# Kernel optimization log

Hardware: AMD Instinct MI355X
Metric: run time of the kernel (lower is better)

## Reference

```python
import jax, jax.numpy as jnp
import numpy as np

B, S, D, H, HID = 8192, 16, 128, 8, 1024
DH = D // H  # 16
GCN, NUMF = 40, 103
EPS = 1e-5

def _make_pe():
    pos = np.arange(S, dtype=np.float64)[:, None]
    i = np.arange(D, dtype=np.float64)[None, :]
    pe = pos / np.power(10000.0, (i // 2 * 2.0) / D)
    pe[:, 0::2] = np.sin(pe[:, 0::2])
    pe[:, 1::2] = np.cos(pe[:, 1::2])
    return jnp.asarray(pe, dtype=jnp.float32)  # [S, D]

PE = _make_pe()

def setup_inputs() -> dict:
    key = jax.random.key(0)
    ks = jax.random.split(key, 16)
    rn = lambda k, shape, s=0.02: (jax.random.normal(k, shape, jnp.float32) * s)
    return {
        "x": jax.random.normal(ks[0], (B, S, D), jnp.float32),
        "gcn_i": jax.random.normal(ks[1], (B, GCN), jnp.float32),
        "num": jax.random.normal(ks[2], (B, NUMF), jnp.float32),
        # two independent encoder layers, params stacked on leading dim
        "Wq": rn(ks[3], (2, D, D)), "bq": jnp.zeros((2, D), jnp.float32),
        "Wk": rn(ks[4], (2, D, D)), "bk": jnp.zeros((2, D), jnp.float32),
        "Wv": rn(ks[5], (2, D, D)), "bv": jnp.zeros((2, D), jnp.float32),
        "Wo": rn(ks[6], (2, D, D)), "bo": jnp.zeros((2, D), jnp.float32),
        "ln1_g": jnp.ones((2, D), jnp.float32), "ln1_b": jnp.zeros((2, D), jnp.float32),
        "W1": rn(ks[7], (2, D, HID)), "b1": jnp.zeros((2, HID), jnp.float32),
        "W2": rn(ks[8], (2, HID, D)), "b2": jnp.zeros((2, D), jnp.float32),
        "ln2_g": jnp.ones((2, D), jnp.float32), "ln2_b": jnp.zeros((2, D), jnp.float32),
        # head
        "Wn": rn(ks[9], (NUMF, D)), "bnum": jnp.zeros((D,), jnp.float32),
        "bn_gamma": jnp.ones((D,), jnp.float32), "bn_beta": jnp.zeros((D,), jnp.float32),
        "Wf": rn(ks[10], (S * D + GCN + D, 1)), "bf": jnp.zeros((1,), jnp.float32),
    }

def _ln(x, g, b):
    m = x.mean(-1, keepdims=True)
    v = ((x - m) ** 2).mean(-1, keepdims=True)
    return (x - m) * jax.lax.rsqrt(v + EPS) * g + b

def reference(x, gcn_i, num, Wq, bq, Wk, bk, Wv, bv, Wo, bo, ln1_g, ln1_b,
              W1, b1, W2, b2, ln2_g, ln2_b, Wn, bnum, bn_gamma, bn_beta, Wf, bf):
    out = x + PE  # positional encoding (dropout = identity in eval)
    scale = DH ** -0.5
    for l in range(2):
        # NOTE: original uses a raw .view(B*H, -1, DH) (no transpose) -- faithful reshape
        q = (out @ Wq[l] + bq[l]).reshape(B * H, S, DH)
        k = (out @ Wk[l] + bk[l]).reshape(B * H, S, DH)
        v = (out @ Wv[l] + bv[l]).reshape(B * H, S, DH)
        attn = jax.nn.softmax(jnp.einsum('nsd,ntd->nst', q, k) * scale, axis=-1)
        ctx = jnp.einsum('nst,ntd->nsd', attn, v).reshape(B, S, D)
        h = _ln(ctx @ Wo[l] + bo[l] + out, ln1_g[l], ln1_b[l])
        ff = jax.nn.relu(h @ W1[l] + b1[l]) @ W2[l] + b2[l]
        out = _ln(ff + h, ln2_g[l], ln2_b[l])
    flat = out.reshape(B, S * D)  # [B, 2048]
    n = num @ Wn + bnum  # [B, 128]
    # BatchNorm1d, training-mode forward (biased batch variance)
    mu = n.mean(0)
    var = ((n - mu) ** 2).mean(0)
    n = (n - mu) * jax.lax.rsqrt(var + EPS) * bn_gamma + bn_beta
    p = jnp.concatenate([flat, gcn_i, n], axis=-1)  # [B, 2216]
    return jax.nn.sigmoid(p @ Wf + bf)
```

## Files before the change

kernel.cpp:

```cpp
#include <hip/hip_runtime.h>
#include <hip/hip_bf16.h>
#include <math.h>

#define B_SZ   8192
#define S_SZ   16
#define D_SZ   128
#define HID_SZ 1024
#define NUMF_SZ 103
#define GCN_SZ 40
#define G_B    4
#define NBLK   (B_SZ / G_B)
#define STRD   136

typedef short bh8 __attribute__((ext_vector_type(8)));
typedef float fx4 __attribute__((ext_vector_type(4)));
typedef unsigned short us4 __attribute__((ext_vector_type(4)));

__device__ __forceinline__ fx4 mfma16(bh8 a, bh8 b, fx4 c) {
    return __builtin_amdgcn_mfma_f32_16x16x32_bf16(a, b, c, 0, 0, 0);
}

__device__ __forceinline__ unsigned short f2b(float f) {
    union { __hip_bfloat16 b; unsigned short u; } cv;
    cv.b = __float2bfloat16(f);
    return cv.u;
}
__device__ __forceinline__ float bu2f(unsigned short u) {
    return __uint_as_float(((unsigned)u) << 16);
}

__global__ __launch_bounds__(256) void prep_weights(
    const float* __restrict__ Wq, const float* __restrict__ Wk,
    const float* __restrict__ Wv, const float* __restrict__ Wo,
    const float* __restrict__ W1, const float* __restrict__ W2,
    unsigned short* __restrict__ WswQ, unsigned short* __restrict__ WswK,
    unsigned short* __restrict__ WswV, unsigned short* __restrict__ WswO,
    unsigned short* __restrict__ Wsw1, unsigned short* __restrict__ Wsw2,
    float* __restrict__ PEt)
{
    int j = blockIdx.x * 256 + threadIdx.x;
    if (j < 2048) {
        int s = j >> 7, c = j & 127;
        float expo = (float)((c >> 1) * 2) * (1.0f / 128.0f);
        float denom = powf(10000.0f, expo);
        float ang = (float)s / denom;
        PEt[j] = (c & 1) ? cosf(ang) : sinf(ang);
    }
    if (j < 2 * 16384) {
        int r = j & 16383, l = j >> 14;
        int k = r >> 7, n = r & 127;
        int dst = (((l * 8 + (n >> 4)) * 4 + (k >> 5)) * 64 +
                   (((k >> 3) & 3) * 16 + (n & 15))) * 8 + (k & 7);
        WswQ[dst] = f2b(Wq[j]); WswK[dst] = f2b(Wk[j]);
        WswV[dst] = f2b(Wv[j]); WswO[dst] = f2b(Wo[j]);
    }
    {
        int l = j >> 17, r = j & 131071;
        int k = r >> 10, n = r & 1023;
        int dst = (((l * 64 + (n >> 4)) * 4 + (k >> 5)) * 64 +
                   (((k >> 3) & 3) * 16 + (n & 15))) * 8 + (k & 7);
        Wsw1[dst] = f2b(W1[j]);
    }
    {
        int l = j >> 17, r = j & 131071;
        int k = r >> 7, n = r & 127;
        int dst = (((l * 8 + (n >> 4)) * 32 + (k >> 5)) * 64 +
                   (((k >> 3) & 3) * 16 + (n & 15))) * 8 + (k & 7);
        Wsw2[dst] = f2b(W2[j]);
    }
}

__global__ __launch_bounds__(256, 2) void encoder_fused(
    const float* __restrict__ x, const float* __restrict__ gcn,
    const float* __restrict__ bq, const float* __restrict__ bk,
    const float* __restrict__ bv, const float* __restrict__ bo,
    const float* __restrict__ ln1g, const float* __restrict__ ln1b,
    const float* __restrict__ b1, const float* __restrict__ b2p,
    const float* __restrict__ ln2g, const float* __restrict__ ln2b,
    const float* __restrict__ Wf,
    const unsigned short* __restrict__ WswQ, const unsigned short* __restrict__ WswK,
    const unsigned short* __restrict__ WswV, const unsigned short* __restrict__ WswO,
    const unsigned short* __restrict__ Wsw1, const unsigned short* __restrict__ Wsw2,
    const float* __restrict__ PEt,
    float* __restrict__ acc1)
{
    __shared__ unsigned short ACT[64][STRD];
    __shared__ unsigned short Qb[64][STRD];
    __shared__ unsigned short Kb[64][STRD];
    __shared__ unsigned short Vb[64][STRD];
    __shared__ float2 LNp2[64][4];
    __shared__ unsigned short Pb[4][16][16];

    unsigned short* Vb4 = &Vb[0][0];

    const int t = threadIdx.x;
    const int w = t >> 6, lane = t & 63;
    const int q = lane >> 4, ln = lane & 15;
    const int bbase = blockIdx.x * G_B;

    {
        const float4* xb = (const float4*)(x + (size_t)bbase * 2048);
        const float4* pe4 = (const float4*)PEt;
#pragma unroll
        for (int i = 0; i < 8; ++i) {
            int f4 = i * 256 + t;
            float4 xv = xb[f4];
            float4 pv = pe4[f4 & 511];
            int flat = f4 * 4;
            int row = flat >> 7, col = flat & 127;
            ushort4 pk = {f2b(xv.x + pv.x), f2b(xv.y + pv.y),
                          f2b(xv.z + pv.z), f2b(xv.w + pv.w)};
            *(ushort4*)&ACT[row][col] = pk;
        }
    }
    __syncthreads();

    for (int l = 0; l < 2; ++l) {
        {
            bh8 afr[4][4];
#pragma unroll
            for (int mt = 0; mt < 4; ++mt)
#pragma unroll
                for (int ks = 0; ks < 4; ++ks)
                    afr[mt][ks] = *(const bh8*)&ACT[mt * 16 + ln][ks * 32 + q * 8];
#pragma unroll
            for (int mtx = 0; mtx < 2; ++mtx) {
                const unsigned short* Wm = (mtx == 0) ? WswQ + l * 16384 : WswK + l * 16384;
                const float* bias = (mtx == 0) ? bq + l * 128 : bk + l * 128;
                unsigned short (*dst)[STRD] = (mtx == 0) ? Qb : Kb;
#pragma unroll
                for (int i2 = 0; i2 < 2; ++i2) {
                    int nt = w * 2 + i2;
                    bh8 wfr[4];
#pragma unroll
                    for (int ks = 0; ks < 4; ++ks)
                        wfr[ks] = *(const bh8*)(Wm + ((nt * 4 + ks) * 64 + lane) * 8);
                    int n0 = nt * 16 + q * 4;
                    fx4 bb4 = *(const fx4*)&bias[n0];
#pragma unroll
                    for (int mt = 0; mt < 4; ++mt) {
                        fx4 acc = {0.f, 0.f, 0.f, 0.f};
#pragma unroll
                        for (int ks = 0; ks < 4; ++ks) acc = mfma16(wfr[ks], afr[mt][ks], acc);
                        us4 o;
#pragma unroll
                        for (int r2 = 0; r2 < 4; ++r2) o[r2] = f2b(acc[r2] + bb4[r2]);
                        *(us4*)&dst[mt * 16 + ln][n0] = o;
                    }
                }
            }
#pragma unroll
            for (int i2 = 0; i2 < 2; ++i2) {
                int nt = w * 2 + i2;
                bh8 wfr[4];
#pragma unroll
                for (int ks = 0; ks < 4; ++ks)
                    wfr[ks] = *(const bh8*)(WswV + l * 16384 + ((nt * 4 + ks) * 64 + lane) * 8);
                int n = nt * 16 + ln;
                float bb = bv[l * 128 + n];
#pragma unroll
                for (int mt = 0; mt < 4; ++mt) {
                    fx4 acc = {0.f, 0.f, 0.f, 0.f};
#pragma unroll
                    for (int ks = 0; ks < 4; ++ks) acc = mfma16(afr[mt][ks], wfr[ks], acc);
#pragma unroll
                    for (int r2 = 0; r2 < 4; ++r2) {
                        int s = q * 4 + r2;
                        Vb4[(((mt * 8 + (s >> 1)) * 16) + ln) * 16 +
                            (((s & 1) << 3) | nt)] = f2b(acc[r2] + bb);
                    }
                }
            }
        }
        __syncthreads();

        {
            const int E = w;
            const int rbase = E * 16 + (ln >> 3);
            const int ccol = (ln & 7) * 16;
#pragma unroll
            for (int g = 0; g < 8; ++g) {
                bh8 kfr = 0, qfr = 0;
                if (q < 2) {
                    kfr = *(const bh8*)&Kb[rbase + 2 * g][ccol + q * 8];
                    qfr = *(const bh8*)&Qb[rbase + 2 * g][ccol + q * 8];
                }
                fx4 st = mfma16(kfr, qfr, fx4{0.f, 0.f, 0.f, 0.f});
                float p0 = st[0] * 0.25f, p1 = st[1] * 0.25f;
                float p2 = st[2] * 0.25f, p3 = st[3] * 0.25f;
                float mx = fmaxf(fmaxf(p0, p1), fmaxf(p2, p3));
                mx = fmaxf(mx, __shfl_xor(mx, 16));
                mx = fmaxf(mx, __shfl_xor(mx, 32));
                p0 = __expf(p0 - mx); p1 = __expf(p1 - mx);
                p2 = __expf(p2 - mx); p3 = __expf(p3 - mx);
                float sm = (p0 + p1) + (p2 + p3);
                sm += __shfl_xor(sm, 16);
                sm += __shfl_xor(sm, 32);
                float is = 1.0f / sm;
                ushort4 pk = {f2b(p0 * is), f2b(p1 * is), f2b(p2 * is), f2b(p3 * is)};
                *(ushort4*)&Pb[w][ln][q * 4] = pk;
                bh8 vfr = 0, pfr = 0;
                if (q < 2) {
                    vfr = *(const bh8*)&Vb4[(((E * 8 + g) * 16) + ln) * 16 + q * 8];
                    pfr = *(const bh8*)&Pb[w][ln][q * 8];
                }
                fx4 cx = mfma16(vfr, pfr, fx4{0.f, 0.f, 0.f, 0.f});
                ushort4 ck = {f2b(cx[0]), f2b(cx[1]), f2b(cx[2]), f2b(cx[3])};
                *(ushort4*)&Qb[rbase + 2 * g][ccol + q * 4] = ck;
            }
        }
        __syncthreads();

        fx4 Cv[2][4];
        {
            bh8 cfr[4][4];
#pragma unroll
            for (int mt = 0; mt < 4; ++mt)
#pragma unroll
                for (int ks = 0; ks < 4; ++ks)
                    cfr[mt][ks] = *(const bh8*)&Qb[mt * 16 + ln][ks * 32 + q * 8];
#pragma unroll
            for (int i2 = 0; i2 < 2; ++i2) {
                int nt = w * 2 + i2, n0 = nt * 16 + q * 4;
                bh8 wfr[4];
#pragma unroll
                for (int ks = 0; ks < 4; ++ks)
                    wfr[ks] = *(const bh8*)(WswO + l * 16384 + ((nt * 4 + ks) * 64 + lane) * 8);
                fx4 bb4 = *(const fx4*)&bo[l * 128 + n0];
#pragma unroll
                for (int mt = 0; mt < 4; ++mt) {
                    fx4 acc = {0.f, 0.f, 0.f, 0.f};
#pragma unroll
                    for (int ks = 0; ks < 4; ++ks) acc = mfma16(wfr[ks], cfr[mt][ks], acc);
                    us4 rv = *(const us4*)&ACT[mt * 16 + ln][n0];
#pragma unroll
                    for (int r2 = 0; r2 < 4; ++r2)
                        Cv[i2][mt][r2] = acc[r2] + bb4[r2] + bu2f(rv[r2]);
                }
            }
        }
#pragma unroll
        for (int mt = 0; mt < 4; ++mt) {
            float s = 0.f, v = 0.f;
#pragma unroll
            for (int i2 = 0; i2 < 2; ++i2)
#pragma unroll
                for (int r2 = 0; r2 < 4; ++r2) {
                    float a = Cv[i2][mt][r2];
                    s += a; v = fmaf(a, a, v);
                }
            s += __shfl_xor(s, 16); v += __shfl_xor(v, 16);
            s += __shfl_xor(s, 32); v += __shfl_xor(v, 32);
            if (lane < 16) LNp2[mt * 16 + ln][w] = float2{s, v};
        }
        __syncthreads();
        {
            float mean4[4], inv4[4];
#pragma unroll
            for (int mt = 0; mt < 4; ++mt) {
                int row = mt * 16 + ln;
                float2 a0 = LNp2[row][0], a1 = LNp2[row][1];
                float2 a2 = LNp2[row][2], a3 = LNp2[row][3];
                float s = (a0.x + a1.x) + (a2.x + a3.x);
                float v = (a0.y + a1.y) + (a2.y + a3.y);
                float mean = s * (1.0f / 128.0f);
                mean4[mt] = mean;
                inv4[mt] = rsqrtf(v * (1.0f / 128.0f) - mean * mean + 1e-5f);
            }
#pragma unroll
            for (int i2 = 0; i2 < 2; ++i2) {
                int n0 = (w * 2 + i2) * 16 + q * 4;
                fx4 gg = *(const fx4*)&ln1g[l * 128 + n0];
                fx4 be = *(const fx4*)&ln1b[l * 128 + n0];
#pragma unroll
                for (int mt = 0; mt < 4; ++mt) {
                    us4 o;
#pragma unroll
                    for (int r2 = 0; r2 < 4; ++r2)
                        o[r2] = f2b((Cv[i2][mt][r2] - mean4[mt]) * inv4[mt] * gg[r2] + be[r2]);
                    *(us4*)&Kb[mt * 16 + ln][n0] = o;
                }
            }
        }
        __syncthreads();

        bh8 hfr[4][4];
#pragma unroll
        for (int mt = 0; mt < 4; ++mt)
#pragma unroll
            for (int ks = 0; ks < 4; ++ks)
                hfr[mt][ks] = *(const bh8*)&Kb[mt * 16 + ln][ks * 32 + q * 8];
        fx4 f2a[2][4];
#pragma unroll
        for (int i2 = 0; i2 < 2; ++i2)
#pragma unroll
            for (int mt = 0; mt < 4; ++mt) f2a[i2][mt] = fx4{0.f, 0.f, 0.f, 0.f};
        for (int ch = 0; ch < 8; ++ch) {
            unsigned short (*dst)[STRD] = (ch & 1) ? Vb : Qb;
            bh8 w1fr[2][4];
#pragma unroll
            for (int i2 = 0; i2 < 2; ++i2) {
                int ntg = ch * 8 + w * 2 + i2;
#pragma unroll
                for (int ks = 0; ks < 4; ++ks)
                    w1fr[i2][ks] = *(const bh8*)(Wsw1 + l * 131072 + ((ntg * 4 + ks) * 64 + lane) * 8);
            }
#pragma unroll
            for (int mt = 0; mt < 4; ++mt) {
#pragma unroll
                for (int i2 = 0; i2 < 2; ++i2) {
                    fx4 acc = {0.f, 0.f, 0.f, 0.f};
#pragma unroll
                    for (int ks = 0; ks < 4; ++ks) acc = mfma16(w1fr[i2][ks], hfr[mt][ks], acc);
                    int nl0 = (w * 2 + i2) * 16 + q * 4;
                    fx4 bb4 = *(const fx4*)&b1[l * HID_SZ + ch * 128 + nl0];
                    us4 o;
#pragma unroll
                    for (int r2 = 0; r2 < 4; ++r2) {
                        float vv = acc[r2] + bb4[r2];
                        o[r2] = f2b(vv > 0.f ? vv : 0.f);
                    }
                    *(us4*)&dst[mt * 16 + ln][nl0] = o;
                }
            }
            __syncthreads();
            bh8 w2fr[2][4];
#pragma unroll
            for (int i2 = 0; i2 < 2; ++i2)
#pragma unroll
                for (int ks = 0; ks < 4; ++ks)
                    w2fr[i2][ks] = *(const bh8*)(Wsw2 + l * 131072 +
                        (((w * 2 + i2) * 32 + ch * 4 + ks) * 64 + lane) * 8);
#pragma unroll
            for (int mt = 0; mt < 4; ++mt) {
                bh8 ffr[4];
#pragma unroll
                for (int ks = 0; ks < 4; ++ks)
                    ffr[ks] = *(const bh8*)&dst[mt * 16 + ln][ks * 32 + q * 8];
#pragma unroll
                for (int i2 = 0; i2 < 2; ++i2)
#pragma unroll
                    for (int ks = 0; ks < 4; ++ks)
                        f2a[i2][mt] = mfma16(w2fr[i2][ks], ffr[ks], f2a[i2][mt]);
            }
        }
        fx4 Cv2[2][4];
#pragma unroll
        for (int i2 = 0; i2 < 2; ++i2) {
            int n0 = (w * 2 + i2) * 16 + q * 4;
            fx4 bb4 = *(const fx4*)&b2p[l * 128 + n0];
#pragma unroll
            for (int mt = 0; mt < 4; ++mt) {
                us4 rv = *(const us4*)&Kb[mt * 16 + ln][n0];
#pragma unroll
                for (int r2 = 0; r2 < 4; ++r2)
                    Cv2[i2][mt][r2] = f2a[i2][mt][r2] + bb4[r2] + bu2f(rv[r2]);
            }
        }
#pragma unroll
        for (int mt = 0; mt < 4; ++mt) {
            float s = 0.f, v = 0.f;
#pragma unroll
            for (int i2 = 0; i2 < 2; ++i2)
#pragma unroll
                for (int r2 = 0; r2 < 4; ++r2) {
                    float a = Cv2[i2][mt][r2];
                    s += a; v = fmaf(a, a, v);
                }
            s += __shfl_xor(s, 16); v += __shfl_xor(v, 16);
            s += __shfl_xor(s, 32); v += __shfl_xor(v, 32);
            if (lane < 16) LNp2[mt * 16 + ln][w] = float2{s, v};
        }
        __syncthreads();
        {
            float mean4[4], inv4[4];
#pragma unroll
            for (int mt = 0; mt < 4; ++mt) {
                int row = mt * 16 + ln;
                float2 a0 = LNp2[row][0], a1 = LNp2[row][1];
                float2 a2 = LNp2[row][2], a3 = LNp2[row][3];
                float s = (a0.x + a1.x) + (a2.x + a3.x);
                float v = (a0.y + a1.y) + (a2.y + a3.y);
                float mean = s * (1.0f / 128.0f);
                mean4[mt] = mean;
                inv4[mt] = rsqrtf(v * (1.0f / 128.0f) - mean * mean + 1e-5f);
            }
#pragma unroll
            for (int i2 = 0; i2 < 2; ++i2) {
                int n0 = (w * 2 + i2) * 16 + q * 4;
                fx4 gg = *(const fx4*)&ln2g[l * 128 + n0];
                fx4 be = *(const fx4*)&ln2b[l * 128 + n0];
#pragma unroll
                for (int mt = 0; mt < 4; ++mt) {
                    us4 o;
#pragma unroll
                    for (int r2 = 0; r2 < 4; ++r2)
                        o[r2] = f2b((Cv2[i2][mt][r2] - mean4[mt]) * inv4[mt] * gg[r2] + be[r2]);
                    *(us4*)&ACT[mt * 16 + ln][n0] = o;
                }
            }
        }
        __syncthreads();
    }

    {
        int bg = bbase + w;
        float part = 0.f;
        int srow = lane >> 2, c0 = (lane & 3) * 32;
#pragma unroll
        for (int i = 0; i < 4; ++i) {
            bh8 av = *(const bh8*)&ACT[w * 16 + srow][c0 + i * 8];
            int fl = srow * 128 + c0 + i * 8;
#pragma unroll
            for (int e = 0; e < 8; ++e)
                part = fmaf(bu2f((unsigned short)av[e]), Wf[fl + e], part);
        }
        if (lane < GCN_SZ)
            part = fmaf(gcn[(size_t)bg * GCN_SZ + lane], Wf[2048 + lane], part);
#pragma unroll
        for (int off = 32; off; off >>= 1) part += __shfl_xor(part, off);
        if (lane == 0) acc1[bg] = part;
    }
}

__global__ __launch_bounds__(256) void num_stats_kernel(
    const float* __restrict__ num, const float* __restrict__ Wn,
    const float* __restrict__ bnum,
    float* __restrict__ ssum, float* __restrict__ ssq)
{
    __shared__ float NUM[16][NUMF_SZ + 1];
    __shared__ float cred[4][128];
    const int t = threadIdx.x;
    const int b0 = blockIdx.x * 16;
    const int j = t & 127, sg = t >> 7, s0 = sg * 8;

    for (int idx = t; idx < 16 * NUMF_SZ; idx += 256) {
        int r = idx / NUMF_SZ, f = idx - r * NUMF_SZ;
        NUM[r][f] = num[(size_t)(b0 + r) * NUMF_SZ + f];
    }
    __syncthreads();

    float acc[8];
    float bnv = bnum[j];
#pragma unroll
    for (int r = 0; r < 8; ++r) acc[r] = bnv;
    for (int f = 0; f < NUMF_SZ; ++f) {
        float w = Wn[f * 128 + j];
#pragma unroll
        for (int r = 0; r < 8; ++r) acc[r] = fmaf(NUM[s0 + r][f], w, acc[r]);
    }
    float lsum = 0.f, lsq = 0.f;
#pragma unroll
    for (int r = 0; r < 8; ++r) {
        lsum += acc[r];
        lsq = fmaf(acc[r], acc[r], lsq);
    }
    cred[sg][j] = lsum;
    cred[2 + sg][j] = lsq;
    __syncthreads();
    if (sg == 0) atomicAdd(&ssum[j], cred[0][j] + cred[1][j]);
    else         atomicAdd(&ssq[j],  cred[2][j] + cred[3][j]);
}

__global__ __launch_bounds__(128) void bn_coef_kernel(
    const float* __restrict__ ssum, const float* __restrict__ ssq,
    const float* __restrict__ gamma, const float* __restrict__ beta,
    const float* __restrict__ Wf, const float* __restrict__ bfin,
    const float* __restrict__ Wn, const float* __restrict__ bnum,
    float* __restrict__ cvec)
{
    const int j = threadIdx.x;
    __shared__ float cS[128];
    __shared__ float red2[2];
    float mean = ssum[j] * (1.0f / (float)B_SZ);
    float var = ssq[j] * (1.0f / (float)B_SZ) - mean * mean;
    float inv = rsqrtf(var + 1e-5f);
    float wj = Wf[2088 + j];
    float gi = gamma[j] * inv;
    float cj = gi * wj;
    cS[j] = cj;
    float k = (beta[j] - mean * gi) * wj + bnum[j] * cj;
#pragma unroll
    for (int o = 32; o; o >>= 1) k += __shfl_down(k, o);
    if ((j & 63) == 0) red2[j >> 6] = k;
    __syncthreads();
    if (j == 0) cvec[103] = red2[0] + red2[1] + bfin[0];
    if (j < NUMF_SZ) {
        float s = 0.f;
        for (int jj = 0; jj < 128; ++jj)
            s = fmaf(Wn[j * 128 + jj], cS[jj], s);
        cvec[j] = s;
    }
}

__global__ __launch_bounds__(256) void final_fast(
    const float* __restrict__ num, const float* __restrict__ cvec,
    const float* __restrict__ acc1, float* __restrict__ out)
{
    __shared__ float wv[104];
    const int t = threadIdx.x;
    if (t < 104) wv[t] = cvec[t];
    __syncthreads();
    const int w = t >> 6, lane = t & 63;
    const int b = blockIdx.x * 4 + w;
    const float* nb = num + (size_t)b * NUMF_SZ;
    float part = nb[lane] * wv[lane];
    if (lane < NUMF_SZ - 64) part += nb[64 + lane] * wv[64 + lane];
#pragma unroll
    for (int o = 32; o; o >>= 1) part += __shfl_xor(part, o);
    if (lane == 0)
        out[b] = 1.0f / (1.0f + __expf(-(acc1[b] + part + wv[103])));
}

extern "C" void kernel_launch(void* const* d_in, const int* in_sizes, int n_in,
                              void* d_out, int out_size, void* d_ws, size_t ws_size,
                              hipStream_t stream)
{
    const float* x    = (const float*)d_in[0];
    const float* gcn  = (const float*)d_in[1];
    const float* num  = (const float*)d_in[2];
    const float* Wq   = (const float*)d_in[3];
    const float* bq   = (const float*)d_in[4];
    const float* Wk   = (const float*)d_in[5];
    const float* bk   = (const float*)d_in[6];
    const float* Wv   = (const float*)d_in[7];
    const float* bv   = (const float*)d_in[8];
    const float* Wo   = (const float*)d_in[9];
    const float* bo   = (const float*)d_in[10];
    const float* ln1g = (const float*)d_in[11];
    const float* ln1b = (const float*)d_in[12];
    const float* W1   = (const float*)d_in[13];
    const float* b1   = (const float*)d_in[14];
    const float* W2   = (const float*)d_in[15];
    const float* b2p  = (const float*)d_in[16];
    const float* ln2g = (const float*)d_in[17];
    const float* ln2b = (const float*)d_in[18];
    const float* Wn   = (const float*)d_in[19];
    const float* bnum = (const float*)d_in[20];
    const float* bng  = (const float*)d_in[21];
    const float* bnb  = (const float*)d_in[22];
    const float* Wf   = (const float*)d_in[23];
    const float* bfin = (const float*)d_in[24];

    float* acc1 = (float*)d_ws;
    float* ssum = acc1 + B_SZ;
    float* ssq  = ssum + 128;
    unsigned short* wb = (unsigned short*)((char*)d_ws + 40960);
    unsigned short* WswQ = wb;
    unsigned short* WswK = wb + 32768;
    unsigned short* WswV = wb + 65536;
    unsigned short* WswO = wb + 98304;
    unsigned short* Wsw1 = wb + 131072;
    unsigned short* Wsw2 = wb + 393216;
    float* PEt = (float*)((char*)d_ws + 40960 + 1310720);
    float* cvec = (float*)((char*)d_ws + 40960 + 1310720 + 8192);

    hipMemsetAsync(ssum, 0, 2 * 128 * sizeof(float), stream);
    prep_weights<<<1024, 256, 0, stream>>>(Wq, Wk, Wv, Wo, W1, W2,
        WswQ, WswK, WswV, WswO, Wsw1, Wsw2, PEt);
    encoder_fused<<<NBLK, 256, 0, stream>>>(x, gcn, bq, bk, bv, bo,
        ln1g, ln1b, b1, b2p, ln2g, ln2b, Wf,
        WswQ, WswK, WswV, WswO, Wsw1, Wsw2, PEt, acc1);
    num_stats_kernel<<<B_SZ / 16, 256, 0, stream>>>(num, Wn, bnum, ssum, ssq);
    bn_coef_kernel<<<1, 128, 0, stream>>>(ssum, ssq, bng, bnb, Wf, bfin,
        Wn, bnum, cvec);
    final_fast<<<B_SZ / 4, 256, 0, stream>>>(num, cvec, acc1, (float*)d_out);
}
```

Measured before the change: 406.0 us.

## Fold BatchNorm stats and coefficient kernels into encoder launch via extra blocks

Adds 512 leading blocks to the encoder launch that compute the num@Wn batch statistics, with a last-block-done atomic counter that then computes the BN-folded coefficient vector. This removes two separate kernel launches and their serialization, and lets the small stats work run alongside the encoder blocks. The cost is extra shared-memory aliasing, an atomic counter that must be zeroed by the widened memset, and a reliance on atomics for cross-block visibility.

```diff
diff --git a/kernel.cpp b/kernel.cpp
--- a/kernel.cpp
+++ b/kernel.cpp
@@ -10,6 +10,7 @@
 #define GCN_SZ 40
 #define G_B    4
 #define NBLK   (B_SZ / G_B)
+#define SBLK   512
 #define STRD   136
 
 typedef short bh8 __attribute__((ext_vector_type(8)));
@@ -82,6 +83,12 @@
     const unsigned short* __restrict__ WswV, const unsigned short* __restrict__ WswO,
     const unsigned short* __restrict__ Wsw1, const unsigned short* __restrict__ Wsw2,
     const float* __restrict__ PEt,
+    const float* __restrict__ num, const float* __restrict__ Wn,
+    const float* __restrict__ bnum,
+    float* __restrict__ ssum, float* __restrict__ ssq,
+    unsigned int* __restrict__ cnt,
+    const float* __restrict__ bng, const float* __restrict__ bnb,
+    const float* __restrict__ bfin, float* __restrict__ cvec,
     float* __restrict__ acc1)
 {
     __shared__ unsigned short ACT[64][STRD];
@@ -90,13 +97,82 @@
     __shared__ unsigned short Vb[64][STRD];
     __shared__ float2 LNp2[64][4];
     __shared__ unsigned short Pb[4][16][16];
+    __shared__ int lastf;
 
     unsigned short* Vb4 = &Vb[0][0];
 
     const int t = threadIdx.x;
     const int w = t >> 6, lane = t & 63;
     const int q = lane >> 4, ln = lane & 15;
-    const int bbase = blockIdx.x * G_B;
+
+    if (blockIdx.x < SBLK) {
+        float* NUMs = (float*)ACT;
+        float* cred = (float*)Qb;
+        float* cS   = (float*)Vb;
+        float* redw = (float*)LNp2;
+        const int b0 = blockIdx.x * 16;
+        const int j = t & 127, sg = t >> 7, s0 = sg * 8;
+
+        for (int idx = t; idx < 16 * NUMF_SZ; idx += 256) {
+            int r = idx / NUMF_SZ, f = idx - r * NUMF_SZ;
+            NUMs[r * 104 + f] = num[(size_t)(b0 + r) * NUMF_SZ + f];
+        }
+        __syncthreads();
+
+        float acc[8];
+        float bnv = bnum[j];
+#pragma unroll
+        for (int r = 0; r < 8; ++r) acc[r] = bnv;
+        for (int f = 0; f < NUMF_SZ; ++f) {
+            float wv = Wn[f * 128 + j];
+#pragma unroll
+            for (int r = 0; r < 8; ++r) acc[r] = fmaf(NUMs[(s0 + r) * 104 + f], wv, acc[r]);
+        }
+        float lsum = 0.f, lsq = 0.f;
+#pragma unroll
+        for (int r = 0; r < 8; ++r) {
+            lsum += acc[r];
+            lsq = fmaf(acc[r], acc[r], lsq);
+        }
+        cred[sg * 128 + j] = lsum;
+        cred[(2 + sg) * 128 + j] = lsq;
+        __syncthreads();
+        if (sg == 0) atomicAdd(&ssum[j], cred[j] + cred[128 + j]);
+        else         atomicAdd(&ssq[j],  cred[256 + j] + cred[384 + j]);
+        __syncthreads();
+        if (t == 0) lastf = (atomicAdd(cnt, 1u) == SBLK - 1u) ? 1 : 0;
+        __syncthreads();
+
+        if (lastf) {
+            float C1p = 0.f;
+            if (t < 128) {
+                float sv = atomicAdd(&ssum[t], 0.f);
+                float qv = atomicAdd(&ssq[t], 0.f);
+                float mean = sv * (1.0f / (float)B_SZ);
+                float var = qv * (1.0f / (float)B_SZ) - mean * mean;
+                float inv = rsqrtf(var + 1e-5f);
+                float wj = Wf[2088 + t];
+                float gi = bng[t] * inv;
+                float cj = gi * wj;
+                cS[t] = cj;
+                C1p = (bnb[t] - mean * gi) * wj + bnum[t] * cj;
+            }
+#pragma unroll
+            for (int o = 32; o; o >>= 1) C1p += __shfl_xor(C1p, o);
+            if (lane == 0) redw[w] = C1p;
+            __syncthreads();
+            if (t == 0) cvec[103] = redw[0] + redw[1] + redw[2] + redw[3] + bfin[0];
+            if (t < NUMF_SZ) {
+                float s2 = 0.f;
+                for (int jj = 0; jj < 128; ++jj)
+                    s2 = fmaf(Wn[t * 128 + jj], cS[jj], s2);
+                cvec[t] = s2;
+            }
+        }
+        return;
+    }
+
+    const int bbase = (blockIdx.x - SBLK) * G_B;
 
     {
         const float4* xb = (const float4*)(x + (size_t)bbase * 2048);
@@ -420,76 +496,6 @@
 #pragma unroll
         for (int off = 32; off; off >>= 1) part += __shfl_xor(part, off);
         if (lane == 0) acc1[bg] = part;
-    }
-}
-
-__global__ __launch_bounds__(256) void num_stats_kernel(
-    const float* __restrict__ num, const float* __restrict__ Wn,
-    const float* __restrict__ bnum,
-    float* __restrict__ ssum, float* __restrict__ ssq)
-{
-    __shared__ float NUM[16][NUMF_SZ + 1];
-    __shared__ float cred[4][128];
-    const int t = threadIdx.x;
-    const int b0 = blockIdx.x * 16;
-    const int j = t & 127, sg = t >> 7, s0 = sg * 8;
-
-    for (int idx = t; idx < 16 * NUMF_SZ; idx += 256) {
-        int r = idx / NUMF_SZ, f = idx - r * NUMF_SZ;
-        NUM[r][f] = num[(size_t)(b0 + r) * NUMF_SZ + f];
-    }
-    __syncthreads();
-
-    float acc[8];
-    float bnv = bnum[j];
-#pragma unroll
-    for (int r = 0; r < 8; ++r) acc[r] = bnv;
-    for (int f = 0; f < NUMF_SZ; ++f) {
-        float w = Wn[f * 128 + j];
-#pragma unroll
-        for (int r = 0; r < 8; ++r) acc[r] = fmaf(NUM[s0 + r][f], w, acc[r]);
-    }
-    float lsum = 0.f, lsq = 0.f;
-#pragma unroll
-    for (int r = 0; r < 8; ++r) {
-        lsum += acc[r];
-        lsq = fmaf(acc[r], acc[r], lsq);
-    }
-    cred[sg][j] = lsum;
-    cred[2 + sg][j] = lsq;
-    __syncthreads();
-    if (sg == 0) atomicAdd(&ssum[j], cred[0][j] + cred[1][j]);
-    else         atomicAdd(&ssq[j],  cred[2][j] + cred[3][j]);
-}
-
-__global__ __launch_bounds__(128) void bn_coef_kernel(
-    const float* __restrict__ ssum, const float* __restrict__ ssq,
-    const float* __restrict__ gamma, const float* __restrict__ beta,
-    const float* __restrict__ Wf, const float* __restrict__ bfin,
-    const float* __restrict__ Wn, const float* __restrict__ bnum,
-    float* __restrict__ cvec)
-{
-    const int j = threadIdx.x;
-    __shared__ float cS[128];
-    __shared__ float red2[2];
-    float mean = ssum[j] * (1.0f / (float)B_SZ);
-    float var = ssq[j] * (1.0f / (float)B_SZ) - mean * mean;
-    float inv = rsqrtf(var + 1e-5f);
-    float wj = Wf[2088 + j];
-    float gi = gamma[j] * inv;
-    float cj = gi * wj;
-    cS[j] = cj;
-    float k = (beta[j] - mean * gi) * wj + bnum[j] * cj;
-#pragma unroll
-    for (int o = 32; o; o >>= 1) k += __shfl_down(k, o);
-    if ((j & 63) == 0) red2[j >> 6] = k;
-    __syncthreads();
-    if (j == 0) cvec[103] = red2[0] + red2[1] + bfin[0];
-    if (j < NUMF_SZ) {
-        float s = 0.f;
-        for (int jj = 0; jj < 128; ++jj)
-            s = fmaf(Wn[j * 128 + jj], cS[jj], s);
-        cvec[j] = s;
     }
 }
 
@@ -545,6 +551,7 @@
     float* acc1 = (float*)d_ws;
     float* ssum = acc1 + B_SZ;
     float* ssq  = ssum + 128;
+    unsigned int* cnt = (unsigned int*)(ssq + 128);
     unsigned short* wb = (unsigned short*)((char*)d_ws + 40960);
     unsigned short* WswQ = wb;
     unsigned short* WswK = wb + 32768;
@@ -555,14 +562,12 @@
     float* PEt = (float*)((char*)d_ws + 40960 + 1310720);
     float* cvec = (float*)((char*)d_ws + 40960 + 1310720 + 8192);
 
-    hipMemsetAsync(ssum, 0, 2 * 128 * sizeof(float), stream);
+    hipMemsetAsync(ssum, 0, 257 * sizeof(float), stream);
     prep_weights<<<1024, 256, 0, stream>>>(Wq, Wk, Wv, Wo, W1, W2,
         WswQ, WswK, WswV, WswO, Wsw1, Wsw2, PEt);
-    encoder_fused<<<NBLK, 256, 0, stream>>>(x, gcn, bq, bk, bv, bo,
+    encoder_fused<<<SBLK + NBLK, 256, 0, stream>>>(x, gcn, bq, bk, bv, bo,
         ln1g, ln1b, b1, b2p, ln2g, ln2b, Wf,
-        WswQ, WswK, WswV, WswO, Wsw1, Wsw2, PEt, acc1);
-    num_stats_kernel<<<B_SZ / 16, 256, 0, stream>>>(num, Wn, bnum, ssum, ssq);
-    bn_coef_kernel<<<1, 128, 0, stream>>>(ssum, ssq, bng, bnb, Wf, bfin,
-        Wn, bnum, cvec);
+        WswQ, WswK, WswV, WswO, Wsw1, Wsw2, PEt,
+        num, Wn, bnum, ssum, ssq, cnt, bng, bnb, bfin, cvec, acc1);
     final_fast<<<B_SZ / 4, 256, 0, stream>>>(num, cvec, acc1, (float*)d_out);
 }
```

After: 403.8 us. Within noise of the previous version (-0.5%).
